# Performance work log

Hardware: AMD Instinct MI355X
Metric: run time of the kernel (lower is better)

## Reference

```python
import jax, jax.numpy as jnp
import numpy as np

N = 200000   # active voxels
C = 64       # channels (INIT_DIM / PLANES[0])
K = 27       # 3^3 kernel offsets for 3D kernel_size=3
M = 100000   # gather/scatter pairs per kernel offset
EPS = 1e-5


def setup_inputs() -> dict:
    key = jax.random.key(0)
    ks = jax.random.split(key, 8)
    x = jax.random.normal(ks[0], (N, C), jnp.float32)
    # kaiming-ish scale for sparse conv kernels [K, Cin, Cout]
    scale = 1.0 / np.sqrt(K * C)
    w1 = jax.random.normal(ks[1], (K, C, C), jnp.float32) * scale
    w2 = jax.random.normal(ks[2], (K, C, C), jnp.float32) * scale
    in_map = jax.random.randint(ks[3], (K, M), 0, N, dtype=jnp.int32)
    out_map = jax.random.randint(ks[4], (K, M), 0, N, dtype=jnp.int32)
    gamma1 = jnp.ones((C,), jnp.float32)
    beta1 = jnp.zeros((C,), jnp.float32)
    mean1 = jax.random.normal(ks[5], (C,), jnp.float32) * 0.1
    var1 = jax.random.uniform(ks[6], (C,), jnp.float32) + 0.5
    gamma2 = jnp.ones((C,), jnp.float32)
    beta2 = jnp.zeros((C,), jnp.float32)
    mean2 = jax.random.normal(ks[7], (C,), jnp.float32) * 0.1
    var2 = jax.random.uniform(jax.random.fold_in(key, 7), (C,), jnp.float32) + 0.5
    return dict(x=x, w1=w1, w2=w2,
                gamma1=gamma1, beta1=beta1, mean1=mean1, var1=var1,
                gamma2=gamma2, beta2=beta2, mean2=mean2, var2=var2,
                in_map=in_map, out_map=out_map)


def sparse_conv(x, w, in_map, out_map):
    """Gather-GEMM-scatter sparse convolution (MinkowskiConvolution core).
    x: [N, Cin]; w: [K, Cin, Cout]; in_map/out_map: [K, M] voxel indices.
    """
    g = x[in_map]                                  # [K, M, Cin] gather
    y = jnp.einsum('kmc,kcd->kmd', g, w)           # per-offset GEMM
    cout = w.shape[-1]
    out = jnp.zeros((N, cout), x.dtype)
    out = out.at[out_map.reshape(-1)].add(y.reshape(-1, cout))  # scatter-add
    return out


def batch_norm(x, gamma, beta, mean, var):
    return (x - mean) * jax.lax.rsqrt(var + EPS) * gamma + beta


def reference(x, w1, w2, gamma1, beta1, mean1, var1,
              gamma2, beta2, mean2, var2, in_map, out_map):
    # BasicBlock: conv1 -> BN -> ReLU -> conv2 -> BN -> +residual -> ReLU
    out = sparse_conv(x, w1, in_map, out_map)
    out = jax.nn.relu(batch_norm(out, gamma1, beta1, mean1, var1))
    out = sparse_conv(out, w2, in_map, out_map)
    out = batch_norm(out, gamma2, beta2, mean2, var2)
    return jax.nn.relu(out + x)
```

## Files before the change

kernel.cpp:

```cpp
#include <hip/hip_runtime.h>
#include <stdint.h>

#define N_VOX    200000
#define C_CH     64
#define K_OFF    27
#define M_PAIRS  100000
#define KM       (K_OFF * M_PAIRS)
#define TILE     64
#define NT       (N_VOX / TILE)
#define NB       (NT * K_OFF)
#define WBN      (K_OFF * 4096)
#define EPS_BN   1e-5f
#define CDCAP    (KM / 16 + NB + 64)

#define SLICES   16
#define SLICE_LEN (M_PAIRS / SLICES)
#define KB       (K_OFF * SLICES)
#define PTS      3200

#define SCHUNK   2048
#define NBLK1    ((NB + SCHUNK - 1) / SCHUNK)
#define PQ1      0
#define PQ2      128

#define YCAP     1040

typedef __attribute__((ext_vector_type(8))) short   short8_t;
typedef __attribute__((ext_vector_type(4))) float   f32x4;

__device__ __forceinline__ unsigned short f2bf(float f) {
    union { float f; unsigned u; } v; v.f = f;
    unsigned r = v.u + 0x7FFFu + ((v.u >> 16) & 1u);
    return (unsigned short)(r >> 16);
}
__device__ __forceinline__ float bf2f(unsigned u16) {
    union { unsigned u; float f; } v; v.u = u16 << 16;
    return v.f;
}
__device__ __forceinline__ int pmap(int cs) {
    int p = cs >> 1, h = cs & 1;
    return (p & 3) * 16 + (p >> 2) * 2 + h;
}

__global__ void prep_kernel(const float* __restrict__ x,
                            const float* __restrict__ w1, const float* __restrict__ w2,
                            const float* __restrict__ g1, const float* __restrict__ b1,
                            const float* __restrict__ m1, const float* __restrict__ v1,
                            const float* __restrict__ g2, const float* __restrict__ b2,
                            const float* __restrict__ m2, const float* __restrict__ v2,
                            unsigned short* __restrict__ xb,
                            unsigned short* __restrict__ wb1, unsigned short* __restrict__ wb2,
                            float* __restrict__ sbp1, float* __restrict__ sbp2)
{
    long i = (long)blockIdx.x * blockDim.x + threadIdx.x;
    const long XBN8 = (long)N_VOX * C_CH / 8;
    if (i < XBN8) {
        const f32x4* sp = (const f32x4*)(x + (size_t)i * 8);
        f32x4 a = sp[0], b = sp[1];
        uint4 o;
        o.x = (unsigned)f2bf(a[0]) | ((unsigned)f2bf(a[1]) << 16);
        o.y = (unsigned)f2bf(a[2]) | ((unsigned)f2bf(a[3]) << 16);
        o.z = (unsigned)f2bf(b[0]) | ((unsigned)f2bf(b[1]) << 16);
        o.w = (unsigned)f2bf(b[2]) | ((unsigned)f2bf(b[3]) << 16);
        ((uint4*)xb)[i] = o;
        return;
    }
    long j = i - XBN8;
    if (j < 2 * WBN) {
        int isw2 = j >= WBN;
        int o = (int)(isw2 ? j - WBN : j);
        int k   = o >> 12;
        int rem = o & 4095;
        int t  = rem >> 11;
        int sl = (rem >> 9) & 3;
        int d  = (rem >> 3) & 63;
        int jj = rem & 7;
        int cs = t * 32 + sl * 8 + jj;
        if (!isw2) wb1[o] = f2bf(w1[k * 4096 + cs * 64 + d]);
        else       wb2[o] = f2bf(w2[k * 4096 + pmap(cs) * 64 + d]);
        return;
    }
    j -= 2 * WBN;
    if (j < 128) {
        int L = (int)(j >= 64);
        int ch = (int)(j & 63);
        float gv = L ? g2[ch] : g1[ch];
        float vv = L ? v2[ch] : v1[ch];
        float mv = L ? m2[ch] : m1[ch];
        float bv = L ? b2[ch] : b1[ch];
        float s = gv * rsqrtf(vv + EPS_BN);
        float sh = bv - mv * s;
        int n = ch >> 4, rem = ch & 15, m = rem >> 1, h = rem & 1;
        int idx = 2 * (m * 4 + n) + h;
        float* sbp = L ? sbp2 : sbp1;
        sbp[idx] = s; sbp[64 + idx] = sh;
    }
}

__global__ __launch_bounds__(256) void hist_kernel(const int* __restrict__ out_map,
                                                   int* __restrict__ partial)
{
    __shared__ int h[3136];
    int blk = blockIdx.x;
    int k = blk >> 4, s = blk & 15;
    int tid = threadIdx.x;
    for (int i = tid; i < 3136; i += 256) h[i] = 0;
    __syncthreads();
    int p0 = k * M_PAIRS + s * SLICE_LEN;
    for (int i = tid; i < SLICE_LEN; i += 256)
        atomicAdd(&h[out_map[p0 + i] >> 6], 1);
    __syncthreads();
    for (int t = tid; t < NT; t += 256)
        partial[blk * PTS + t] = h[t];
}

__global__ __launch_bounds__(256) void transp_kernel(const int* __restrict__ partial,
                                                     int* __restrict__ partial_T)
{
    __shared__ int tb[32][33];
    int bx = blockIdx.x % 14, by = blockIdx.x / 14;
    int kb0 = bx * 32, t0 = by * 32;
    int tx = threadIdx.x & 31, ty = threadIdx.x >> 5;
    #pragma unroll
    for (int dy = 0; dy < 32; dy += 8) {
        int kb = kb0 + ty + dy;
        tb[ty + dy][tx] = (kb < KB) ? partial[kb * PTS + t0 + tx] : 0;
    }
    __syncthreads();
    #pragma unroll
    for (int dy = 0; dy < 32; dy += 8) {
        int t = t0 + ty + dy;
        int kb = kb0 + tx;
        if (t < NT && kb < KB)
            partial_T[t * KB + kb] = tb[tx][ty + dy];
    }
}

__global__ __launch_bounds__(256) void scanA_kernel(const int* __restrict__ partial_T,
                                                    int* __restrict__ part)
{
    __shared__ int lds[256], lds2[256];
    int b0 = blockIdx.x * SCHUNK;
    int t = threadIdx.x;
    int sraw = 0, sc16 = 0;
    for (int i = t; i < SCHUNK; i += 256) {
        int b = b0 + i;
        if (b < NB) {
            int tt = b / K_OFF, k = b % K_OFF;
            const int* pr = &partial_T[tt * KB + k * SLICES];
            int c = 0;
            #pragma unroll
            for (int s = 0; s < SLICES; ++s) c += pr[s];
            sraw += c; sc16 += (c + 15) >> 4;
        }
    }
    lds[t] = sraw; lds2[t] = sc16;
    __syncthreads();
    for (int d = 128; d > 0; d >>= 1) {
        if (t < d) { lds[t] += lds[t + d]; lds2[t] += lds2[t + d]; }
        __syncthreads();
    }
    if (t == 0) { part[PQ1 + blockIdx.x] = lds[0]; part[PQ2 + blockIdx.x] = lds2[0]; }
}

__global__ __launch_bounds__(128) void scanB_kernel(int* __restrict__ part) {
    __shared__ int lds[128];
    int g = blockIdx.x, t = threadIdx.x;
    int base = (g == 0) ? PQ1 : PQ2;
    int v = (t < NBLK1) ? part[base + t] : 0;
    lds[t] = v;
    __syncthreads();
    for (int d = 1; d < 128; d <<= 1) {
        int u = (t >= d) ? lds[t - d] : 0;
        __syncthreads();
        lds[t] += u;
        __syncthreads();
    }
    if (t < NBLK1) part[base + t] = lds[t] - v;
}

__global__ __launch_bounds__(256) void scanC_kernel(const int* __restrict__ partial_T,
                                                    const int* __restrict__ part,
                                                    int* __restrict__ offs,
                                                    int* __restrict__ cdoffs,
                                                    int* __restrict__ base)
{
    __shared__ int lds[256], lds2[256];
    int b = blockIdx.x, t = threadIdx.x;
    int i0 = b * SCHUNK + t * 8;
    int c[8]; int sraw = 0, sc16 = 0;
    #pragma unroll
    for (int j = 0; j < 8; ++j) {
        int idx = i0 + j;
        int tot = 0;
        if (idx < NB) {
            int tt = idx / K_OFF, k = idx - tt * K_OFF;
            const int* pr = &partial_T[tt * KB + k * SLICES];
            #pragma unroll
            for (int s = 0; s < SLICES; ++s) tot += pr[s];
        }
        c[j] = tot;
        sraw += tot; sc16 += (tot + 15) >> 4;
    }
    int vr = sraw, vc = sc16;
    lds[t] = vr; lds2[t] = vc;
    __syncthreads();
    for (int d = 1; d < 256; d <<= 1) {
        int ur = (t >= d) ? lds[t - d] : 0;
        int uc = (t >= d) ? lds2[t - d] : 0;
        __syncthreads();
        lds[t] += ur; lds2[t] += uc;
        __syncthreads();
    }
    int braw = part[PQ1 + b] + lds[t] - vr;
    int bc16 = part[PQ2 + b] + lds2[t] - vc;
    #pragma unroll
    for (int j = 0; j < 8; ++j) {
        int idx = i0 + j;
        if (idx < NB) {
            offs[idx] = braw; cdoffs[idx] = bc16;
            int tt = idx / K_OFF, k = idx - tt * K_OFF;
            const int* pr = &partial_T[tt * KB + k * SLICES];
            int run = braw;
            #pragma unroll
            for (int s = 0; s < SLICES; ++s) {
                base[(k * SLICES + s) * PTS + tt] = run;
                run += pr[s];
            }
        }
        braw += c[j]; bc16 += (c[j] + 15) >> 4;
    }
    if (b == NBLK1 - 1 && t == 255) { offs[NB] = braw; cdoffs[NB] = bc16; }
}

__global__ __launch_bounds__(256) void scatter2_kernel(const int* __restrict__ in_map,
                                                       const int* __restrict__ out_map,
                                                       const int* __restrict__ base,
                                                       unsigned* __restrict__ pp)
{
    __shared__ int lbase[NT];
    __shared__ int h2[NT];
    int blk = blockIdx.x;
    int k = blk >> 4, s = blk & 15;
    int tid = threadIdx.x;
    const int* gb = &base[(k * SLICES + s) * PTS];
    for (int i = tid; i < NT; i += 256) { lbase[i] = gb[i]; h2[i] = 0; }
    __syncthreads();
    int p0 = k * M_PAIRS + s * SLICE_LEN;
    #pragma unroll 2
    for (int i = tid; i < SLICE_LEN; i += 256) {
        int p = p0 + i;
        int o = out_map[p];
        int t = o >> 6;
        int rank = atomicAdd(&h2[t], 1);
        pp[lbase[t] + rank] = (unsigned)in_map[p] | ((unsigned)(o & 63) << 18);
    }
}

__global__ void cdescb_kernel(const int* __restrict__ offs, const int* __restrict__ cdoffs,
                              unsigned long long* __restrict__ cdesc)
{
    int b = blockIdx.x * 256 + threadIdx.x;
    if (b >= NB) return;
    int k = b % K_OFF;
    int c0 = cdoffs[b];
    int nchunk = cdoffs[b + 1] - c0;
    int base = offs[b];
    int end  = offs[b + 1];
    for (int i = 0; i < nchunk; ++i)
        cdesc[c0 + i] = (unsigned long long)k
                      | ((unsigned long long)(base + 16 * i) << 5)
                      | ((unsigned long long)end << 27);
}

template<int LAYER>
__global__ __launch_bounds__(1024, 1) void fused_kernel(
    const unsigned short* __restrict__ xin,
    const unsigned short* __restrict__ wb,
    const unsigned* __restrict__ pp,
    const unsigned long long* __restrict__ cdesc,
    const int* __restrict__ offs,
    const int* __restrict__ cdoffs,
    const float* __restrict__ sbp,
    const float* __restrict__ xres,
    void* __restrict__ outp)
{
    __shared__ unsigned Ylds[(YCAP + 8) * 32];
    __shared__ unsigned short ridx[YCAP];
    __shared__ unsigned short rrank[YCAP];
    __shared__ unsigned char  soloc[YCAP];
    __shared__ int hist[TILE];
    __shared__ int cstart[TILE + 1];

    const int tile = blockIdx.x;
    const int tid = threadIdx.x;
    const int p0 = offs[tile * K_OFF];
    const int p1 = offs[(tile + 1) * K_OFF];
    const int c0 = cdoffs[tile * K_OFF];
    const int c1 = cdoffs[(tile + 1) * K_OFF];
    int nr = p1 - p0; if (nr > YCAP) nr = YCAP;

    if (tid < TILE) hist[tid] = 0;
    __syncthreads();
    for (int i = tid; i < nr; i += 1024) {
        int ol = (int)((pp[p0 + i] >> 18) & 63);
        soloc[i] = (unsigned char)ol;
        rrank[i] = (unsigned short)atomicAdd(&hist[ol], 1);
    }
    __syncthreads();
    if (tid < 64) {
        int v = hist[tid];
        int s = v;
        #pragma unroll
        for (int d = 1; d < 64; d <<= 1) {
            int u = __shfl_up(s, d, 64);
            if (tid >= d) s += u;
        }
        cstart[tid] = s - v;
        if (tid == 63) cstart[64] = s;
    }
    __syncthreads();
    for (int i = tid; i < nr; i += 1024)
        ridx[cstart[soloc[i]] + rrank[i]] = (unsigned short)i;

    const int wid   = tid >> 6;
    const int lane  = tid & 63;
    const int r     = lane & 15;
    const int sfour = lane >> 4;
    const int par   = lane & 1;

    for (int c = c0 + wid; c < c1; c += 16) {
        unsigned long long d = cdesc[c];
        int k     = (int)(d & 31);
        int pbase = (int)((d >> 5) & 0x3FFFFF);
        int pend  = (int)(d >> 27);

        int ii = pbase + r;
        bool real = ii < pend;
        unsigned pv = pp[real ? ii : pbase];
        unsigned iidx = pv & 0x3FFFFu;
        int yr;
        if (real) { yr = ii - p0; if (yr > YCAP) yr = YCAP; }
        else      { yr = YCAP + (c & 7); }

        const short8_t* xrow = (const short8_t*)(xin + (size_t)iidx * 64);
        short8_t A0 = xrow[sfour];
        short8_t A1 = xrow[4 + sfour];
        const short8_t* wbk = (const short8_t*)(wb + k * 4096);

        f32x4 acc[4] = {{0,0,0,0},{0,0,0,0},{0,0,0,0},{0,0,0,0}};
        #pragma unroll
        for (int n = 0; n < 4; ++n) {
            acc[n] = __builtin_amdgcn_mfma_f32_16x16x32_bf16(A0, wbk[sfour * 64 + n * 16 + r], acc[n], 0, 0, 0);
            acc[n] = __builtin_amdgcn_mfma_f32_16x16x32_bf16(A1, wbk[(4 + sfour) * 64 + n * 16 + r], acc[n], 0, 0, 0);
        }

        #pragma unroll
        for (int jj = 0; jj < 4; jj += 2) {
            uint4 w;
            unsigned* wp = (unsigned*)&w;
            #pragma unroll
            for (int n = 0; n < 4; ++n) {
                float mine = par ? acc[n][jj + 1] : acc[n][jj];
                float send = par ? acc[n][jj]     : acc[n][jj + 1];
                float tt = __shfl_xor(send, 1, 64);
                float lo = par ? tt : mine;
                float hi = par ? mine : tt;
                wp[n] = (unsigned)f2bf(lo) | ((unsigned)f2bf(hi) << 16);
            }
            int Rw = sfour * 4 + jj + par;
            int yrow = __shfl(yr, Rw, 64);
            *(uint4*)&Ylds[(unsigned)yrow * 32 + (r >> 1) * 4] = w;
        }
    }
    __syncthreads();

    const int v  = tid >> 4;
    const int q2 = tid & 15;
    int cs0 = cstart[v], cs1 = cstart[v + 1];
    float sum[4] = {0.f, 0.f, 0.f, 0.f};
    for (int j = cs0; j < cs1; ++j) {
        int row = (int)ridx[j];
        uint2 u = *(const uint2*)&Ylds[(unsigned)row * 32 + 2 * q2];
        sum[0] += bf2f(u.x & 0xFFFFu);
        sum[1] += bf2f(u.x >> 16);
        sum[2] += bf2f(u.y & 0xFFFFu);
        sum[3] += bf2f(u.y >> 16);
    }

    const int og = tile * TILE + v;
    const float2* sc2 = (const float2*)sbp;
    const float2* sh2 = (const float2*)(sbp + 64);
    int pA = 2 * q2, pB = 2 * q2 + 1;
    float a0 = sum[0] * sc2[pA].x + sh2[pA].x;
    float a1 = sum[1] * sc2[pA].y + sh2[pA].y;
    float b0 = sum[2] * sc2[pB].x + sh2[pB].x;
    float b1 = sum[3] * sc2[pB].y + sh2[pB].y;
    if (LAYER == 0) {
        a0 = a0 > 0.f ? a0 : 0.f; a1 = a1 > 0.f ? a1 : 0.f;
        b0 = b0 > 0.f ? b0 : 0.f; b1 = b1 > 0.f ? b1 : 0.f;
        uint2 o2;
        o2.x = (unsigned)f2bf(a0) | ((unsigned)f2bf(a1) << 16);
        o2.y = (unsigned)f2bf(b0) | ((unsigned)f2bf(b1) << 16);
        *(uint2*)((unsigned*)outp + (size_t)og * 32 + 2 * q2) = o2;
    } else {
        float* out = (float*)outp;
        int chA = (pA & 3) * 16 + (pA >> 2) * 2;
        int chB = (pB & 3) * 16 + (pB >> 2) * 2;
        float2 xrA = *(const float2*)(xres + (size_t)og * 64 + chA);
        float2 xrB = *(const float2*)(xres + (size_t)og * 64 + chB);
        a0 += xrA.x; a1 += xrA.y; b0 += xrB.x; b1 += xrB.y;
        a0 = a0 > 0.f ? a0 : 0.f; a1 = a1 > 0.f ? a1 : 0.f;
        b0 = b0 > 0.f ? b0 : 0.f; b1 = b1 > 0.f ? b1 : 0.f;
        *(float2*)(out + (size_t)og * 64 + chA) = make_float2(a0, a1);
        *(float2*)(out + (size_t)og * 64 + chB) = make_float2(b0, b1);
    }
}

extern "C" void kernel_launch(void* const* d_in, const int* in_sizes, int n_in,
                              void* d_out, int out_size, void* d_ws, size_t ws_size,
                              hipStream_t stream)
{
    const float* x  = (const float*)d_in[0];
    const float* w1 = (const float*)d_in[1];
    const float* w2 = (const float*)d_in[2];
    const float* g1 = (const float*)d_in[3];
    const float* b1 = (const float*)d_in[4];
    const float* m1 = (const float*)d_in[5];
    const float* v1 = (const float*)d_in[6];
    const float* g2 = (const float*)d_in[7];
    const float* b2 = (const float*)d_in[8];
    const float* m2 = (const float*)d_in[9];
    const float* v2 = (const float*)d_in[10];
    const int* in_map  = (const int*)d_in[11];
    const int* out_map = (const int*)d_in[12];

    char* ws = (char*)d_ws;
    size_t off = 0;
    auto alloc = [&](size_t bytes) -> void* {
        void* p = ws + off;
        off = (off + bytes + 255) & ~(size_t)255;
        return p;
    };
    int* partial   = (int*)alloc((size_t)KB * PTS * 4);
    int* partial_T = (int*)alloc((size_t)NT * KB * 4);
    int* base      = (int*)alloc((size_t)KB * PTS * 4);
    int* offs      = (int*)alloc((size_t)(NB + 1) * 4);
    int* cdoffs    = (int*)alloc((size_t)(NB + 1) * 4);
    int* part      = (int*)alloc(512 * 4);
    float* sbp1    = (float*)alloc(128 * 4);
    float* sbp2    = (float*)alloc(128 * 4);
    unsigned short* wb1 = (unsigned short*)alloc((size_t)WBN * 2);
    unsigned short* wb2 = (unsigned short*)alloc((size_t)WBN * 2);
    unsigned* pp   = (unsigned*)alloc((size_t)KM * 4);
    unsigned long long* cdesc = (unsigned long long*)alloc((size_t)CDCAP * 8);
    unsigned short* xb = (unsigned short*)alloc((size_t)N_VOX * C_CH * 2);
    unsigned short* hb = (unsigned short*)alloc((size_t)N_VOX * C_CH * 2);

    const long TOT = (long)N_VOX * C_CH / 8 + 2 * WBN + 128;
    prep_kernel<<<(int)((TOT + 255) / 256), 256, 0, stream>>>(
        x, w1, w2, g1, b1, m1, v1, g2, b2, m2, v2,
        xb, wb1, wb2, sbp1, sbp2);

    hist_kernel<<<KB, 256, 0, stream>>>(out_map, partial);
    transp_kernel<<<14 * ((NT + 31) / 32), 256, 0, stream>>>(partial, partial_T);
    scanA_kernel<<<NBLK1, 256, 0, stream>>>(partial_T, part);
    scanB_kernel<<<2, 128, 0, stream>>>(part);
    scanC_kernel<<<NBLK1, 256, 0, stream>>>(partial_T, part, offs, cdoffs, base);
    scatter2_kernel<<<KB, 256, 0, stream>>>(in_map, out_map, base, pp);
    cdescb_kernel<<<(NB + 255) / 256, 256, 0, stream>>>(offs, cdoffs, cdesc);

    fused_kernel<0><<<NT, 1024, 0, stream>>>(xb, wb1, pp, cdesc, offs, cdoffs,
                                             sbp1, nullptr, hb);
    fused_kernel<1><<<NT, 1024, 0, stream>>>(hb, wb2, pp, cdesc, offs, cdoffs,
                                             sbp2, x, d_out);
}
```

Measured before the change: 467.9 us.

## Prefetch chunk gathers two-deep with contiguous per-wave chunks and cached weights

Chunk descriptors and pair entries are staged in LDS, and each wave now takes a contiguous range of chunks instead of a strided one. Gathers of input rows are software-pipelined two chunks ahead so their global-load latency overlaps the MFMA work. Weight fragments are reloaded only when the kernel offset changes, and bf16 packing uses the hardware cvt_pk instruction. The cost is more LDS and register pressure. The contiguous split can also unbalance waves, and the hardware rounding may differ slightly from the manual round-to-nearest-even.

Result: faster. 397.6 us (median of 2 runs) (-15.0%).

```diff
diff --git a/kernel.cpp b/kernel.cpp
--- a/kernel.cpp
+++ b/kernel.cpp
@@ -24,6 +24,7 @@
 #define PQ2      128
 
 #define YCAP     1040
+#define CLCAP    160
 
 typedef __attribute__((ext_vector_type(8))) short   short8_t;
 typedef __attribute__((ext_vector_type(4))) float   f32x4;
@@ -286,6 +287,8 @@
     void* __restrict__ outp)
 {
     __shared__ unsigned Ylds[(YCAP + 8) * 32];
+    __shared__ unsigned ppl[YCAP];
+    __shared__ unsigned long long cl[CLCAP];
     __shared__ unsigned short ridx[YCAP];
     __shared__ unsigned short rrank[YCAP];
     __shared__ unsigned char  soloc[YCAP];
@@ -298,12 +301,16 @@
     const int p1 = offs[(tile + 1) * K_OFF];
     const int c0 = cdoffs[tile * K_OFF];
     const int c1 = cdoffs[(tile + 1) * K_OFF];
+    const int nch = c1 - c0;
     int nr = p1 - p0; if (nr > YCAP) nr = YCAP;
 
+    for (int i = tid; i < nch && i < CLCAP; i += 1024) cl[i] = cdesc[c0 + i];
     if (tid < TILE) hist[tid] = 0;
     __syncthreads();
     for (int i = tid; i < nr; i += 1024) {
-        int ol = (int)((pp[p0 + i] >> 18) & 63);
+        unsigned pv = pp[p0 + i];
+        ppl[i] = pv;
+        int ol = (int)((pv >> 18) & 63);
         soloc[i] = (unsigned char)ol;
         rrank[i] = (unsigned short)atomicAdd(&hist[ol], 1);
     }
@@ -329,50 +336,83 @@
     const int sfour = lane >> 4;
     const int par   = lane & 1;
 
-    for (int c = c0 + wid; c < c1; c += 16) {
-        unsigned long long d = cdesc[c];
-        int k     = (int)(d & 31);
-        int pbase = (int)((d >> 5) & 0x3FFFFF);
-        int pend  = (int)(d >> 27);
-
-        int ii = pbase + r;
-        bool real = ii < pend;
-        unsigned pv = pp[real ? ii : pbase];
-        unsigned iidx = pv & 0x3FFFFu;
-        int yr;
-        if (real) { yr = ii - p0; if (yr > YCAP) yr = YCAP; }
-        else      { yr = YCAP + (c & 7); }
-
-        const short8_t* xrow = (const short8_t*)(xin + (size_t)iidx * 64);
-        short8_t A0 = xrow[sfour];
-        short8_t A1 = xrow[4 + sfour];
-        const short8_t* wbk = (const short8_t*)(wb + k * 4096);
-
-        f32x4 acc[4] = {{0,0,0,0},{0,0,0,0},{0,0,0,0},{0,0,0,0}};
-        #pragma unroll
-        for (int n = 0; n < 4; ++n) {
-            acc[n] = __builtin_amdgcn_mfma_f32_16x16x32_bf16(A0, wbk[sfour * 64 + n * 16 + r], acc[n], 0, 0, 0);
-            acc[n] = __builtin_amdgcn_mfma_f32_16x16x32_bf16(A1, wbk[(4 + sfour) * 64 + n * 16 + r], acc[n], 0, 0, 0);
-        }
-
-        #pragma unroll
-        for (int jj = 0; jj < 4; jj += 2) {
-            uint4 w;
-            unsigned* wp = (unsigned*)&w;
-            #pragma unroll
-            for (int n = 0; n < 4; ++n) {
-                float mine = par ? acc[n][jj + 1] : acc[n][jj];
-                float send = par ? acc[n][jj]     : acc[n][jj + 1];
-                float tt = __shfl_xor(send, 1, 64);
-                float lo = par ? tt : mine;
-                float hi = par ? mine : tt;
-                wp[n] = (unsigned)f2bf(lo) | ((unsigned)f2bf(hi) << 16);
-            }
-            int Rw = sfour * 4 + jj + par;
-            int yrow = __shfl(yr, Rw, 64);
-            *(uint4*)&Ylds[(unsigned)yrow * 32 + (r >> 1) * 4] = w;
-        }
-    }
+    const int CPW = (nch + 15) >> 4;
+    int w0 = wid * CPW; if (w0 > nch) w0 = nch;
+    int w1 = w0 + CPW;  if (w1 > nch) w1 = nch;
+
+    short8_t A0s[2], A1s[2];
+    int yrs[2], kks[2];
+    short8_t B0[4], B1[4];
+    int kcur = -1;
+
+#define ISSUE(S, CI) do {                                                     \
+        int _ci = (CI);                                                       \
+        if (_ci < w1) {                                                       \
+            unsigned long long _d = (_ci < CLCAP) ? cl[_ci] : cdesc[c0 + _ci];\
+            kks[S] = (int)(_d & 31);                                          \
+            int _pbr = (int)((_d >> 5) & 0x3FFFFF) - p0;                      \
+            int _per = (int)(_d >> 27) - p0;                                  \
+            int _ii = _pbr + r;                                               \
+            bool _real = _ii < _per;                                          \
+            int _idx = _real ? _ii : _pbr;                                    \
+            if (_idx >= YCAP) _idx = 0;                                       \
+            unsigned _pv = ppl[_idx];                                         \
+            yrs[S] = (_real && _ii < YCAP) ? _ii : (YCAP + (_ci & 7));        \
+            const short8_t* _xr =                                             \
+                (const short8_t*)(xin + (size_t)(_pv & 0x3FFFFu) * 64);       \
+            A0s[S] = _xr[sfour];                                              \
+            A1s[S] = _xr[4 + sfour];                                          \
+        }                                                                     \
+    } while (0)
+
+#define CONSUME(S) do {                                                       \
+        int _kk = kks[S];                                                     \
+        if (_kk != kcur) {                                                    \
+            kcur = _kk;                                                       \
+            const short8_t* _wbk = (const short8_t*)(wb + kcur * 4096);       \
+            _Pragma("unroll")                                                 \
+            for (int n = 0; n < 4; ++n) {                                     \
+                B0[n] = _wbk[sfour * 64 + n * 16 + r];                        \
+                B1[n] = _wbk[(4 + sfour) * 64 + n * 16 + r];                  \
+            }                                                                 \
+        }                                                                     \
+        f32x4 acc[4] = {{0,0,0,0},{0,0,0,0},{0,0,0,0},{0,0,0,0}};             \
+        _Pragma("unroll")                                                     \
+        for (int n = 0; n < 4; ++n) {                                         \
+            acc[n] = __builtin_amdgcn_mfma_f32_16x16x32_bf16(A0s[S], B0[n], acc[n], 0, 0, 0); \
+            acc[n] = __builtin_amdgcn_mfma_f32_16x16x32_bf16(A1s[S], B1[n], acc[n], 0, 0, 0); \
+        }                                                                     \
+        int _yr = yrs[S];                                                     \
+        _Pragma("unroll")                                                     \
+        for (int jj = 0; jj < 4; jj += 2) {                                   \
+            uint4 _w;                                                         \
+            unsigned* _wp = (unsigned*)&_w;                                   \
+            _Pragma("unroll")                                                 \
+            for (int n = 0; n < 4; ++n) {                                     \
+                float _mine = par ? acc[n][jj + 1] : acc[n][jj];              \
+                float _send = par ? acc[n][jj]     : acc[n][jj + 1];          \
+                float _t = __shfl_xor(_send, 1, 64);                          \
+                float _lo = par ? _t : _mine;                                 \
+                float _hi = par ? _mine : _t;                                 \
+                unsigned _pk;                                                 \
+                asm("v_cvt_pk_bf16_f32 %0, %1, %2" : "=v"(_pk) : "v"(_lo), "v"(_hi)); \
+                _wp[n] = _pk;                                                 \
+            }                                                                 \
+            int _Rw = sfour * 4 + jj + par;                                   \
+            int _yrow = __shfl(_yr, _Rw, 64);                                 \
+            *(uint4*)&Ylds[(unsigned)_yrow * 32 + (r >> 1) * 4] = _w;         \
+        }                                                                     \
+    } while (0)
+
+    ISSUE(0, w0);
+    ISSUE(1, w0 + 1);
+    #pragma unroll 1
+    for (int i = w0; i < w1; i += 2) {
+        CONSUME(0); ISSUE(0, i + 2);
+        if (i + 1 < w1) { CONSUME(1); ISSUE(1, i + 3); }
+    }
+#undef ISSUE
+#undef CONSUME
     __syncthreads();
 
     const int v  = tid >> 4;
```
